# Optimization experiments

Measured on AMD Instinct MI355X. Metric: run time of the kernel, lower is better.

The kernel has to match this reference:

```python
import jax, jax.numpy as jnp
import numpy as np

DIST_THD = 1.0   # config.dist_thd
EPS = 1e-8       # matches torch.nn.functional.cosine_similarity eps


def setup_inputs() -> dict:
    key = jax.random.key(0)
    k1, k2 = jax.random.split(key)
    async_fea = jax.random.normal(k1, (64, 512, 128), dtype=jnp.float32)  # [B, N, D]
    coord = jax.random.normal(k2, (64, 512, 2), dtype=jnp.float32)        # [B, N, 2]
    return {"async_fea": async_fea, "coord": coord}


def reference(async_fea, coord):
    B, N, _ = async_fea.shape
    # pairwise cosine similarity: normalize rows, then batched matmul
    norms = jnp.maximum(jnp.linalg.norm(async_fea, axis=-1, keepdims=True), EPS)
    fn = async_fea / norms
    cos = jnp.einsum('bid,bjd->bij', fn, fn)  # [B, N, N]

    # pairwise euclidean distance on coords
    diff = coord[:, :, None, :] - coord[:, None, :, :]  # [B, N, N, 2]
    d2 = jnp.sum(diff * diff, axis=-1)                   # [B, N, N]
    eye = jnp.eye(N, dtype=d2.dtype)
    # add eye before sqrt so the (zeroed-out) diagonal stays sqrt-safe
    dist = jnp.sqrt(d2 + eye)
    off_diag = 1.0 - eye

    async_adj = cos * jnp.exp(-dist / DIST_THD) * off_diag
    sync_adj = jnp.where(dist < DIST_THD, 1.0, 0.0) * off_diag
    return jnp.stack([async_adj, sync_adj])  # [2, B, N, N]
```

## Files before the change

### kernel.cpp

```cpp
#include <hip/hip_runtime.h>
#include <hip/hip_bf16.h>

typedef short bf16x8 __attribute__((ext_vector_type(8)));
typedef float f32x4  __attribute__((ext_vector_type(4)));

#define NB 64
#define NN 512
#define DD 128

__device__ __forceinline__ unsigned short f2bf(float f) {
    unsigned int u = __float_as_uint(f);
    unsigned int r = (u + 0x7FFFu + ((u >> 16) & 1u)) >> 16;
    return (unsigned short)r;
}

__global__ __launch_bounds__(256) void ASG_norm_kernel(
    const float* __restrict__ fea, unsigned int* __restrict__ fn)
{
    const int wid  = threadIdx.x >> 6;
    const int lane = threadIdx.x & 63;
    const int row0 = blockIdx.x * 16 + wid * 4;
    const float2* src = reinterpret_cast<const float2*>(fea);

    float2 v[4];
    float  s[4];
#pragma unroll
    for (int rr = 0; rr < 4; ++rr) {
        v[rr] = src[(size_t)(row0 + rr) * (DD / 2) + lane];
        s[rr] = v[rr].x * v[rr].x + v[rr].y * v[rr].y;
    }
#pragma unroll
    for (int o = 32; o; o >>= 1) {
#pragma unroll
        for (int rr = 0; rr < 4; ++rr) s[rr] += __shfl_xor(s[rr], o);
    }
#pragma unroll
    for (int rr = 0; rr < 4; ++rr) {
        const float scale = 1.0f / fmaxf(sqrtf(s[rr]), 1e-8f);
        const unsigned short a = f2bf(v[rr].x * scale);
        const unsigned short b = f2bf(v[rr].y * scale);
        fn[(size_t)(row0 + rr) * (DD / 2) + lane] =
            (unsigned int)a | ((unsigned int)b << 16);
    }
}

__global__ __launch_bounds__(256) void ASG_adj_kernel(
    const unsigned short* __restrict__ fn, const float* __restrict__ coord,
    float* __restrict__ out)
{
    const int id  = blockIdx.x;
    const int xcd = id & 7;
    const int q   = id >> 3;
    const int b   = xcd + 8 * (q >> 4);
    const int t   = q & 15;
    const int bi  = t >> 2;
    const int bj  = t & 3;

    const int tid = threadIdx.x;
    const int wid = tid >> 6, lane = tid & 63;
    const int wr  = wid >> 1, wc = wid & 1;
    const int row0 = bi * 128 + wr * 64;
    const int col0 = bj * 128 + wc * 64;
    const int lo = lane & 15, hi = lane >> 4;

    __shared__ float2 crow[128];
    __shared__ float2 ccol[128];
    __shared__ float  xpose[4][16 * 68];

    const float2* cb = reinterpret_cast<const float2*>(coord) + (size_t)b * NN;
    if (tid < 128) crow[tid] = cb[bi * 128 + tid];
    else           ccol[tid - 128] = cb[bj * 128 + (tid - 128)];
    __syncthreads();

    const unsigned short* fb = fn + (size_t)b * NN * DD;
    const int lk = hi * 8;

    bf16x8 bfrag[4][4];
#pragma unroll
    for (int n = 0; n < 4; ++n) {
        const unsigned short* p = fb + (size_t)(col0 + n * 16 + lo) * DD + lk;
#pragma unroll
        for (int kk = 0; kk < 4; ++kk)
            bfrag[n][kk] = *reinterpret_cast<const bf16x8*>(p + kk * 32);
    }

    f32x4 acc[4][4];
#pragma unroll
    for (int m = 0; m < 4; ++m)
#pragma unroll
        for (int n = 0; n < 4; ++n)
            acc[m][n] = (f32x4){0.f, 0.f, 0.f, 0.f};

#pragma unroll
    for (int m = 0; m < 4; ++m) {
        const unsigned short* p = fb + (size_t)(row0 + m * 16 + lo) * DD + lk;
        bf16x8 afrag[4];
#pragma unroll
        for (int kk = 0; kk < 4; ++kk)
            afrag[kk] = *reinterpret_cast<const bf16x8*>(p + kk * 32);
#pragma unroll
        for (int n = 0; n < 4; ++n)
#pragma unroll
            for (int kk = 0; kk < 4; ++kk)
                acc[m][n] = __builtin_amdgcn_mfma_f32_16x16x32_bf16(
                    afrag[kk], bfrag[n][kk], acc[m][n], 0, 0, 0);
    }

    float* outA = out + (size_t)b * NN * NN;
    float* outS = out + (size_t)NB * NN * NN + (size_t)b * NN * NN;
    float* xp = xpose[wid];

    const int jbase = col0 + lo * 4;
    float2 cj[4];
#pragma unroll
    for (int q2 = 0; q2 < 4; ++q2) cj[q2] = ccol[wc * 64 + lo * 4 + q2];

#pragma unroll
    for (int m = 0; m < 4; ++m) {
#pragma unroll
        for (int n = 0; n < 4; ++n)
#pragma unroll
            for (int r = 0; r < 4; ++r)
                xp[(hi * 4 + r) * 68 + n * 16 + lo] = acc[m][n][r];
#pragma unroll
        for (int p = 0; p < 4; ++p) {
            const int rr = p * 4 + hi;
            const f32x4 cv = *reinterpret_cast<const f32x4*>(&xp[rr * 68 + lo * 4]);
            const int i = row0 + m * 16 + rr;
            const float2 ci = crow[wr * 64 + m * 16 + rr];
            f32x4 av, sv;
#pragma unroll
            for (int q2 = 0; q2 < 4; ++q2) {
                const int j = jbase + q2;
                const float dx = ci.x - cj[q2].x;
                const float dy = ci.y - cj[q2].y;
                const float d2 = __fadd_rn(__fmul_rn(dx, dx), __fmul_rn(dy, dy));
                const float dist = __fsqrt_rn(d2);
                const bool diag = (i == j);
                av[q2] = diag ? 0.0f : cv[q2] * __expf(-dist);
                sv[q2] = (!diag && dist < 1.0f) ? 1.0f : 0.0f;
            }
            const size_t off = (size_t)i * NN + jbase;
            __builtin_nontemporal_store(av, reinterpret_cast<f32x4*>(outA + off));
            __builtin_nontemporal_store(sv, reinterpret_cast<f32x4*>(outS + off));
        }
    }
}

extern "C" void kernel_launch(void* const* d_in, const int* in_sizes, int n_in,
                              void* d_out, int out_size, void* d_ws, size_t ws_size,
                              hipStream_t stream) {
    const float* fea   = (const float*)d_in[0];
    const float* coord = (const float*)d_in[1];
    float* out = (float*)d_out;
    unsigned int* fn_ws = (unsigned int*)d_ws;

    ASG_norm_kernel<<<dim3(NB * NN / 16), 256, 0, stream>>>(fea, fn_ws);
    ASG_adj_kernel<<<dim3(4 * 4 * NB), 256, 0, stream>>>(
        (const unsigned short*)fn_ws, coord, out);
}
```

Measured before the change: 44.47 us.

## Halve adj kernel column tile and interleave MMA with epilogue per row block

The adjacency kernel's tile shrinks from 128x128 to 128x64, doubling the grid to 2048 blocks. Each warp now computes one 16-row block's products and writes it out before moving on, so only two accumulators are live at a time instead of sixteen. Together with launch_bounds(256,4) this cuts register pressure and aims for higher occupancy and better overlap of the output stores. The cost is rereading A fragments twice as often across blocks and narrower 128-byte row segments per store.

Result: faster. 41.77 us (-6.1%).

```diff
diff --git a/kernel.cpp b/kernel.cpp
--- a/kernel.cpp
+++ b/kernel.cpp
@@ -44,52 +44,55 @@
     }
 }
 
-__global__ __launch_bounds__(256) void ASG_adj_kernel(
+__global__ __launch_bounds__(256, 4) void ASG_adj_kernel(
     const unsigned short* __restrict__ fn, const float* __restrict__ coord,
     float* __restrict__ out)
 {
     const int id  = blockIdx.x;
     const int xcd = id & 7;
     const int q   = id >> 3;
-    const int b   = xcd + 8 * (q >> 4);
-    const int t   = q & 15;
-    const int bi  = t >> 2;
-    const int bj  = t & 3;
+    const int b   = xcd + 8 * (q >> 5);
+    const int t   = q & 31;
+    const int bi  = t >> 3;
+    const int bj  = t & 7;
 
     const int tid = threadIdx.x;
     const int wid = tid >> 6, lane = tid & 63;
     const int wr  = wid >> 1, wc = wid & 1;
     const int row0 = bi * 128 + wr * 64;
-    const int col0 = bj * 128 + wc * 64;
+    const int col0 = bj * 64  + wc * 32;
     const int lo = lane & 15, hi = lane >> 4;
 
     __shared__ float2 crow[128];
-    __shared__ float2 ccol[128];
-    __shared__ float  xpose[4][16 * 68];
+    __shared__ float2 ccol[64];
+    __shared__ float  xpose[4][16 * 36];
 
     const float2* cb = reinterpret_cast<const float2*>(coord) + (size_t)b * NN;
-    if (tid < 128) crow[tid] = cb[bi * 128 + tid];
-    else           ccol[tid - 128] = cb[bj * 128 + (tid - 128)];
+    if (tid < 128)      crow[tid] = cb[bi * 128 + tid];
+    else if (tid < 192) ccol[tid - 128] = cb[bj * 64 + (tid - 128)];
     __syncthreads();
 
     const unsigned short* fb = fn + (size_t)b * NN * DD;
     const int lk = hi * 8;
 
-    bf16x8 bfrag[4][4];
+    bf16x8 bfrag[2][4];
 #pragma unroll
-    for (int n = 0; n < 4; ++n) {
+    for (int n = 0; n < 2; ++n) {
         const unsigned short* p = fb + (size_t)(col0 + n * 16 + lo) * DD + lk;
 #pragma unroll
         for (int kk = 0; kk < 4; ++kk)
             bfrag[n][kk] = *reinterpret_cast<const bf16x8*>(p + kk * 32);
     }
 
-    f32x4 acc[4][4];
+    float* outA = out + (size_t)b * NN * NN;
+    float* outS = out + (size_t)NB * NN * NN + (size_t)b * NN * NN;
+    float* xp = xpose[wid];
+
+    const int c4 = (lane & 7) * 4;
+    const int jbase = col0 + c4;
+    float2 cj[4];
 #pragma unroll
-    for (int m = 0; m < 4; ++m)
-#pragma unroll
-        for (int n = 0; n < 4; ++n)
-            acc[m][n] = (f32x4){0.f, 0.f, 0.f, 0.f};
+    for (int q2 = 0; q2 < 4; ++q2) cj[q2] = ccol[wc * 32 + c4 + q2];
 
 #pragma unroll
     for (int m = 0; m < 4; ++m) {
@@ -98,34 +101,27 @@
 #pragma unroll
         for (int kk = 0; kk < 4; ++kk)
             afrag[kk] = *reinterpret_cast<const bf16x8*>(p + kk * 32);
+
+        f32x4 acc[2];
 #pragma unroll
-        for (int n = 0; n < 4; ++n)
+        for (int n = 0; n < 2; ++n) acc[n] = (f32x4){0.f, 0.f, 0.f, 0.f};
+#pragma unroll
+        for (int n = 0; n < 2; ++n)
 #pragma unroll
             for (int kk = 0; kk < 4; ++kk)
-                acc[m][n] = __builtin_amdgcn_mfma_f32_16x16x32_bf16(
-                    afrag[kk], bfrag[n][kk], acc[m][n], 0, 0, 0);
-    }
-
-    float* outA = out + (size_t)b * NN * NN;
-    float* outS = out + (size_t)NB * NN * NN + (size_t)b * NN * NN;
-    float* xp = xpose[wid];
-
-    const int jbase = col0 + lo * 4;
-    float2 cj[4];
-#pragma unroll
-    for (int q2 = 0; q2 < 4; ++q2) cj[q2] = ccol[wc * 64 + lo * 4 + q2];
+                acc[n] = __builtin_amdgcn_mfma_f32_16x16x32_bf16(
+                    afrag[kk], bfrag[n][kk], acc[n], 0, 0, 0);
 
 #pragma unroll
-    for (int m = 0; m < 4; ++m) {
-#pragma unroll
-        for (int n = 0; n < 4; ++n)
+        for (int n = 0; n < 2; ++n)
 #pragma unroll
             for (int r = 0; r < 4; ++r)
-                xp[(hi * 4 + r) * 68 + n * 16 + lo] = acc[m][n][r];
+                xp[(hi * 4 + r) * 36 + n * 16 + lo] = acc[n][r];
+
 #pragma unroll
-        for (int p = 0; p < 4; ++p) {
-            const int rr = p * 4 + hi;
-            const f32x4 cv = *reinterpret_cast<const f32x4*>(&xp[rr * 68 + lo * 4]);
+        for (int p2 = 0; p2 < 2; ++p2) {
+            const int rr = p2 * 8 + (lane >> 3);
+            const f32x4 cv = *reinterpret_cast<const f32x4*>(&xp[rr * 36 + c4]);
             const int i = row0 + m * 16 + rr;
             const float2 ci = crow[wr * 64 + m * 16 + rr];
             f32x4 av, sv;
@@ -156,6 +152,6 @@
     unsigned int* fn_ws = (unsigned int*)d_ws;
 
     ASG_norm_kernel<<<dim3(NB * NN / 16), 256, 0, stream>>>(fea, fn_ws);
-    ASG_adj_kernel<<<dim3(4 * 4 * NB), 256, 0, stream>>>(
+    ASG_adj_kernel<<<dim3(4 * 8 * NB), 256, 0, stream>>>(
         (const unsigned short*)fn_ws, coord, out);
 }
```
